# Performance work log

Hardware: AMD Instinct MI355X
Metric: run time of the kernel (lower is better)

## Reference

```python
import jax, jax.numpy as jnp
import numpy as np

B, T, D = 2, 2048, 1024
QH, KVH = 16, 4
HD = D // QH          # 64
G = QH // KVH         # group size 4
SCALE = HD ** -0.5


def _rope_rotate(x):
    # interleaved rotation: (x1, x2) -> (-x2, x1)
    x1 = x[..., ::2]
    x2 = x[..., 1::2]
    return jnp.stack((-x2, x1), axis=-1).reshape(x.shape)


def setup_inputs() -> dict:
    key = jax.random.key(0)
    k0, k1, k2, k3 = jax.random.split(key, 4)
    x = jax.random.normal(k0, (B, T, D), dtype=jnp.float32)
    # proper RoPE tables, shape [T, HD], each frequency repeated for the interleaved pair
    inv_freq = 1.0 / (10000.0 ** (np.arange(0, HD, 2, dtype=np.float32) / HD))
    freqs = np.arange(T, dtype=np.float32)[:, None] * inv_freq[None, :]   # [T, HD/2]
    freqs = np.repeat(freqs, 2, axis=-1)                                   # [T, HD]
    cos = jnp.asarray(np.cos(freqs), dtype=jnp.float32)
    sin = jnp.asarray(np.sin(freqs), dtype=jnp.float32)
    # glorot-uniform weights stored torch-style as [out, in]
    def glorot(k, out_d, in_d):
        lim = float(np.sqrt(6.0 / (in_d + out_d)))
        return jax.random.uniform(k, (out_d, in_d), jnp.float32, -lim, lim)
    Wq = glorot(k1, D, D)
    Wkv = glorot(k2, 2 * KVH * HD, D)
    Wo = glorot(k3, D, D)
    return {"x": x, "cos": cos, "sin": sin, "Wq": Wq, "Wkv": Wkv, "Wo": Wo}


def reference(x, cos, sin, Wq, Wkv, Wo):
    # projections (torch Linear: y = x @ W.T)
    q = (x @ Wq.T).reshape(B, T, QH, HD).transpose(0, 2, 1, 3)        # [B,QH,T,HD]
    kv = (x @ Wkv.T).reshape(B, T, KVH, 2, HD)
    k = kv[..., 0, :].transpose(0, 2, 1, 3)                            # [B,KVH,T,HD]
    v = kv[..., 1, :].transpose(0, 2, 1, 3)                            # [B,KVH,T,HD]
    # inline RoPE (cos/sin broadcast over batch & heads)
    q = q * cos + _rope_rotate(q) * sin
    k = k * cos + _rope_rotate(k) * sin
    # GQA via broadcast instead of repeat_interleave (same math)
    qg = q.reshape(B, KVH, G, T, HD)
    scores = jnp.einsum('bkgtd,bksd->bkgts', qg, k) * SCALE            # [B,KVH,G,T,T]
    attn = jax.nn.softmax(scores, axis=-1)  # dropout is identity in eval
    out = jnp.einsum('bkgts,bksd->bkgtd', attn, v)                     # [B,KVH,G,T,HD]
    out = out.reshape(B, QH, T, HD).transpose(0, 2, 1, 3).reshape(B, T, D)
    return out @ Wo.T
```

## Files before the change

### kernel.cpp

```cpp
#include <hip/hip_runtime.h>


typedef __bf16 bf16x8 __attribute__((ext_vector_type(8)));
typedef float f32x4 __attribute__((ext_vector_type(4)));
typedef float f32x16 __attribute__((ext_vector_type(16)));
typedef int i32x4 __attribute__((ext_vector_type(4)));
typedef unsigned short ushort4v __attribute__((ext_vector_type(4)));
typedef unsigned short ushort8v __attribute__((ext_vector_type(8)));
typedef unsigned short u16;
typedef unsigned int u32;

#define DEVINL __device__ __forceinline__

DEVINL float bf2f(u16 u) {
  unsigned int x = ((unsigned int)u) << 16;
  return __builtin_bit_cast(float, x);
}
DEVINL u16 f2bf(float f) {
  unsigned int x = __builtin_bit_cast(unsigned int, f);
  x += 0x7fffu + ((x >> 16) & 1u);
  return (u16)(x >> 16);
}
DEVINL float exp2r(float x) {
  float r;
  asm("v_exp_f32 %0, %1" : "=v"(r) : "v"(x));
  return r;
}

constexpr int Bb = 2, Tt = 2048, Dd = 1024, QH = 16, KVH = 4, HD = 64;
constexpr float SCALE_L2E = 0.125f * 1.44269504088896340736f;
constexpr int KVSZ = 131072;

__global__ void cvt_all(const float* __restrict__ x, const float* __restrict__ Wq,
                        const float* __restrict__ Wkv, const float* __restrict__ Wo,
                        u16* __restrict__ xb, u16* __restrict__ wqkv,
                        u16* __restrict__ wob) {
  int i = blockIdx.x * 256 + threadIdx.x;
  const float* src;
  u16* dst;
  if (i < 1048576) {
    src = x; dst = xb;
  } else if (i < 1310720) {
    src = Wq - (size_t)1048576 * 4; dst = wqkv - (size_t)1048576 * 4;
  } else if (i < 1441792) {
    src = Wkv - (size_t)1310720 * 4; dst = wqkv + (size_t)1024 * 1024 - (size_t)1310720 * 4;
  } else {
    src = Wo - (size_t)1441792 * 4; dst = wob - (size_t)1441792 * 4;
  }
  float4 v = reinterpret_cast<const float4*>(src)[i];
  ushort4v o = {f2bf(v.x), f2bf(v.y), f2bf(v.z), f2bf(v.w)};
  *reinterpret_cast<ushort4v*>(dst + (size_t)i * 4) = o;
}

template <bool OUT_F32>
__global__ __launch_bounds__(256) void gemm_bt(const u16* __restrict__ A,
                                               const u16* __restrict__ Bw,
                                               void* __restrict__ Cout, int M, int N, int K) {
  __shared__ alignas(16) u16 lA[128 * 64];
  __shared__ alignas(16) u16 lB[128 * 64];
  const int tid = threadIdx.x;
  const int w = tid >> 6, lane = tid & 63;
  const int r16 = lane & 15, g4 = lane >> 4;
  const int row0 = blockIdx.y * 128, col0 = blockIdx.x * 128;
  const int sr = tid >> 3, sc = tid & 7;
  const int NT = K >> 6;

  bf16x8 ra[4], rb[4];
  f32x4 acc[4][4];
#pragma unroll
  for (int i = 0; i < 4; ++i)
#pragma unroll
    for (int j = 0; j < 4; ++j) acc[i][j] = f32x4{0.f, 0.f, 0.f, 0.f};

  const int wm = (w >> 1) * 64, wn = (w & 1) * 64;

#pragma unroll
  for (int i = 0; i < 4; ++i) {
    int r = i * 32 + sr;
    ra[i] = *reinterpret_cast<const bf16x8*>(A + (size_t)(row0 + r) * K + sc * 8);
    rb[i] = *reinterpret_cast<const bf16x8*>(Bw + (size_t)(col0 + r) * K + sc * 8);
  }

  for (int kt = 0; kt < NT; ++kt) {
    __syncthreads();
#pragma unroll
    for (int i = 0; i < 4; ++i) {
      int r = i * 32 + sr;
      int c = (sc ^ (r & 7)) * 8;
      *reinterpret_cast<bf16x8*>(&lA[r * 64 + c]) = ra[i];
      *reinterpret_cast<bf16x8*>(&lB[r * 64 + c]) = rb[i];
    }
    __syncthreads();
    if (kt + 1 < NT) {
      int k0 = (kt + 1) << 6;
#pragma unroll
      for (int i = 0; i < 4; ++i) {
        int r = i * 32 + sr;
        ra[i] = *reinterpret_cast<const bf16x8*>(A + (size_t)(row0 + r) * K + k0 + sc * 8);
        rb[i] = *reinterpret_cast<const bf16x8*>(Bw + (size_t)(col0 + r) * K + k0 + sc * 8);
      }
    }
#pragma unroll
    for (int kk = 0; kk < 2; ++kk) {
      bf16x8 af[4], bfr[4];
#pragma unroll
      for (int mf = 0; mf < 4; ++mf) {
        int r = wm + mf * 16 + r16;
        int c = ((kk * 4 + g4) ^ (r & 7)) * 8;
        af[mf] = *reinterpret_cast<const bf16x8*>(&lA[r * 64 + c]);
      }
#pragma unroll
      for (int nf = 0; nf < 4; ++nf) {
        int r = wn + nf * 16 + r16;
        int c = ((kk * 4 + g4) ^ (r & 7)) * 8;
        bfr[nf] = *reinterpret_cast<const bf16x8*>(&lB[r * 64 + c]);
      }
#pragma unroll
      for (int mf = 0; mf < 4; ++mf)
#pragma unroll
        for (int nf = 0; nf < 4; ++nf)
          acc[mf][nf] =
              __builtin_amdgcn_mfma_f32_16x16x32_bf16(af[mf], bfr[nf], acc[mf][nf], 0, 0, 0);
    }
  }

#pragma unroll
  for (int mf = 0; mf < 4; ++mf)
#pragma unroll
    for (int nf = 0; nf < 4; ++nf)
#pragma unroll
      for (int r = 0; r < 4; ++r) {
        size_t row = (size_t)(row0 + wm + mf * 16 + g4 * 4 + r);
        size_t col = (size_t)(col0 + wn + nf * 16 + r16);
        float v = acc[mf][nf][r];
        if (OUT_F32)
          reinterpret_cast<float*>(Cout)[row * N + col] = v;
        else
          reinterpret_cast<u16*>(Cout)[row * N + col] = f2bf(v);
      }
}

__global__ void rope_scatter(const u16* __restrict__ P, const float* __restrict__ cosT,
                             const float* __restrict__ sinT, u16* __restrict__ Q,
                             u16* __restrict__ Kc) {
  int idx = blockIdx.x * 256 + threadIdx.x;
  if (idx >= (Bb * Tt) * 640) return;
  int row = idx / 640, p = idx - row * 640;
  int b = row >> 11, t = row & 2047;
  int n, d;
  u16* outp;
  float scl;
  if (p < 512) {
    n = p * 2;
    int h = n >> 6;
    d = n & 63;
    outp = Q + ((size_t)(b * QH + h) * Tt + t) * HD + d;
    scl = SCALE_L2E;
  } else {
    int r2 = p - 512;
    int kvh = r2 >> 5, dp = r2 & 31;
    d = dp * 2;
    n = 1024 + kvh * 128 + d;
    int bh = b * KVH + kvh;
    int kf = d >> 4, h8 = (d >> 3) & 1, j = d & 7;
    outp = Kc + (size_t)bh * KVSZ + ((t >> 5) * 4 + kf) * 512 + (h8 * 32 + (t & 31)) * 8 + j;
    scl = 1.0f;
  }
  unsigned int pv = *reinterpret_cast<const unsigned int*>(P + (size_t)row * 1536 + n);
  float v0 = bf2f((u16)(pv & 0xffffu)), v1 = bf2f((u16)(pv >> 16));
  float c = cosT[t * HD + d], s = sinT[t * HD + d];
  float o0 = (v0 * c - v1 * s) * scl;
  float o1 = (v1 * c + v0 * s) * scl;
  unsigned int ob = (unsigned int)f2bf(o0) | ((unsigned int)f2bf(o1) << 16);
  *reinterpret_cast<unsigned int*>(outp) = ob;
}

__global__ void v_transpose(const u16* __restrict__ P, u16* __restrict__ Vf) {
  __shared__ u16 tile[64][72];
  int bh = blockIdx.y;
  int b = bh >> 2, kvh = bh & 3;
  int t0 = blockIdx.x * 64;
  int tid = threadIdx.x;
  int colbase = 1024 + kvh * 128 + 64;
#pragma unroll
  for (int j = 0; j < 4; ++j) {
    int rr = j * 16 + (tid >> 4);
    int cc = (tid & 15) * 4;
    *reinterpret_cast<uint2*>(&tile[rr][cc]) =
        *reinterpret_cast<const uint2*>(P + (size_t)(b * Tt + t0 + rr) * 1536 + colbase + cc);
  }
  __syncthreads();
#pragma unroll
  for (int kk = 0; kk < 2; ++kk) {
    int CH = kk * 256 + tid;
    int df = CH >> 8, sbks = (CH >> 6) & 3, h8 = (CH >> 5) & 1, l = CH & 31;
    int d = df * 32 + l;
    int c = (sbks >> 1) * 4 + (sbks & 1) * 2 + h8;
    ushort8v v;
#pragma unroll
    for (int j = 0; j < 8; ++j) v[j] = tile[c * 8 + j][d];
    u16* dst = Vf + (size_t)bh * KVSZ + (((t0 >> 6) * 2 + df) * 4 + sbks) * 512 +
               (h8 * 32 + l) * 8;
    *reinterpret_cast<ushort8v*>(dst) = v;
  }
}

__global__ __launch_bounds__(512, 4) void attn_fwd7(const u16* __restrict__ Q,
                                                    const u16* __restrict__ Kf,
                                                    const u16* __restrict__ Vf,
                                                    u16* __restrict__ Oa) {
  __shared__ alignas(16) float cmb[2][32][66];
  __shared__ alignas(16) u16 ot[2][32][72];
  const int tid = threadIdx.x;
  const int w = tid >> 6, lane = tid & 63;
  const int qsub = w & 1, spl = w >> 1;
  const int l31 = lane & 31, hi = lane >> 5;

  const int fid = blockIdx.x;
  const int xcd = fid & 7, idx = fid >> 3;
  const int b = xcd >> 2, kvh = xcd & 3;
  const int g = idx & 3, qblk = idx >> 2;
  const int h = kvh * 4 + g;
  const int t0 = qblk * 64 + qsub * 32;

  const u16* Qh = Q + ((size_t)(b * QH + h) * Tt + t0 + l31) * HD + hi * 8;
  const u16* Kp = Kf + (size_t)(b * KVH + kvh) * KVSZ + lane * 8 + (size_t)spl * 32768;
  const u16* Vp = Vf + (size_t)(b * KVH + kvh) * KVSZ + lane * 8 + (size_t)spl * 32768;

  bf16x8 qf[4];
#pragma unroll
  for (int kf = 0; kf < 4; ++kf)
    qf[kf] = *reinterpret_cast<const bf16x8*>(Qh + kf * 16);

  f32x16 oacc[2];
#pragma unroll
  for (int df = 0; df < 2; ++df)
#pragma unroll
    for (int r = 0; r < 16; ++r) oacc[df][r] = 0.f;
  float lp = 0.f;

  for (int it = 0; it < 8; ++it, Kp += 4096, Vp += 4096) {
    f32x16 sacc[2];
#pragma unroll
    for (int sb = 0; sb < 2; ++sb) {
      bf16x8 kfr[4];
#pragma unroll
      for (int kf = 0; kf < 4; ++kf)
        kfr[kf] = *reinterpret_cast<const bf16x8*>(Kp + sb * 2048 + kf * 512);
#pragma unroll
      for (int r = 0; r < 16; ++r) sacc[sb][r] = 0.f;
      __builtin_amdgcn_s_setprio(1);
#pragma unroll
      for (int kf = 0; kf < 4; ++kf)
        sacc[sb] = __builtin_amdgcn_mfma_f32_32x32x16_bf16(kfr[kf], qf[kf], sacc[sb], 0, 0, 0);
      __builtin_amdgcn_s_setprio(0);
    }

    float a0 = 0.f, a1 = 0.f, a2 = 0.f, a3 = 0.f;
#pragma unroll
    for (int sb = 0; sb < 2; ++sb)
#pragma unroll
      for (int r = 0; r < 16; r += 4) {
        float e0 = exp2r(sacc[sb][r]);
        float e1 = exp2r(sacc[sb][r + 1]);
        float e2 = exp2r(sacc[sb][r + 2]);
        float e3 = exp2r(sacc[sb][r + 3]);
        sacc[sb][r] = e0; sacc[sb][r + 1] = e1; sacc[sb][r + 2] = e2; sacc[sb][r + 3] = e3;
        a0 += e0; a1 += e1; a2 += e2; a3 += e3;
      }
    lp += (a0 + a1) + (a2 + a3);

    bf16x8 pf[2][2];
#pragma unroll
    for (int sb = 0; sb < 2; ++sb) {
      u32 pw[8];
#pragma unroll
      for (int r2 = 0; r2 < 8; ++r2) {
        u32 o;
        asm("v_cvt_pk_bf16_f32 %0, %1, %2"
            : "=v"(o)
            : "v"(sacc[sb][2 * r2]), "v"(sacc[sb][2 * r2 + 1]));
        pw[r2] = o;
      }
      u32 fw[2][4];
#pragma unroll
      for (int pp = 0; pp < 4; ++pp) {
        int ks = pp >> 1, o = pp & 1;
        u32 a = pw[ks * 4 + o], bq = pw[ks * 4 + o + 2];
        asm("v_permlane32_swap_b32 %0, %1" : "+v"(a), "+v"(bq));
        fw[ks][o] = a;
        fw[ks][o + 2] = bq;
      }
#pragma unroll
      for (int ks = 0; ks < 2; ++ks) {
        i32x4 iv = {(int)fw[ks][0], (int)fw[ks][1], (int)fw[ks][2], (int)fw[ks][3]};
        pf[sb][ks] = __builtin_bit_cast(bf16x8, iv);
      }
    }

    bf16x8 vf[2][2][2];
#pragma unroll
    for (int df = 0; df < 2; ++df)
#pragma unroll
      for (int sb = 0; sb < 2; ++sb)
#pragma unroll
        for (int ks = 0; ks < 2; ++ks)
          vf[df][sb][ks] =
              *reinterpret_cast<const bf16x8*>(Vp + (size_t)(df * 4 + sb * 2 + ks) * 512);

    __builtin_amdgcn_s_setprio(1);
#pragma unroll
    for (int df = 0; df < 2; ++df)
#pragma unroll
      for (int sb = 0; sb < 2; ++sb)
#pragma unroll
        for (int ks = 0; ks < 2; ++ks)
          oacc[df] =
              __builtin_amdgcn_mfma_f32_32x32x16_bf16(vf[df][sb][ks], pf[sb][ks], oacc[df], 0, 0, 0);
    __builtin_amdgcn_s_setprio(0);
  }

  lp += __shfl_xor(lp, 32);

  for (int src = 1; src < 4; ++src) {
    if (spl == src) {
      float* cb = &cmb[qsub][l31][0];
#pragma unroll
      for (int df = 0; df < 2; ++df)
#pragma unroll
        for (int r = 0; r < 16; ++r) {
          int d = df * 32 + (r & 3) + 8 * (r >> 2) + 4 * hi;
          cb[d] = oacc[df][r];
        }
      if (hi == 0) cb[64] = lp;
    }
    __syncthreads();
    if (spl == 0) {
      const float* cb = &cmb[qsub][l31][0];
      lp += cb[64];
#pragma unroll
      for (int df = 0; df < 2; ++df)
#pragma unroll
        for (int r = 0; r < 16; ++r) {
          int d = df * 32 + (r & 3) + 8 * (r >> 2) + 4 * hi;
          oacc[df][r] += cb[d];
        }
    }
    __syncthreads();
  }

  if (spl == 0) {
    float linv = 1.0f / lp;
#pragma unroll
    for (int df = 0; df < 2; ++df)
#pragma unroll
      for (int r = 0; r < 16; ++r) {
        int d = df * 32 + (r & 3) + 8 * (r >> 2) + 4 * hi;
        ot[qsub][l31][d] = f2bf(oacc[df][r] * linv);
      }
  }
  __syncthreads();
  if (spl == 0) {
    int tr = lane >> 1, dblk = (lane & 1) * 32;
    u16* gdst = Oa + ((size_t)(b * Tt + t0 + tr)) * Dd + h * HD + dblk;
#pragma unroll
    for (int c = 0; c < 4; ++c) {
      ushort8v vv = *reinterpret_cast<const ushort8v*>(&ot[qsub][tr][dblk + c * 8]);
      *reinterpret_cast<ushort8v*>(gdst + c * 8) = vv;
    }
  }
}

extern "C" void kernel_launch(void* const* d_in, const int* in_sizes, int n_in, void* d_out,
                              int out_size, void* d_ws, size_t ws_size, hipStream_t stream) {
  (void)in_sizes; (void)n_in; (void)out_size; (void)ws_size;
  const float* x = (const float*)d_in[0];
  const float* cosT = (const float*)d_in[1];
  const float* sinT = (const float*)d_in[2];
  const float* Wq = (const float*)d_in[3];
  const float* Wkv = (const float*)d_in[4];
  const float* Wo = (const float*)d_in[5];

  char* p = (char*)d_ws;
  u16* xb = (u16*)p;   p += (size_t)4096 * 1024 * 2;
  u16* wqkv = (u16*)p; p += (size_t)1536 * 1024 * 2;
  u16* wob = (u16*)p;  p += (size_t)1024 * 1024 * 2;
  u16* Pbuf = (u16*)p; p += (size_t)4096 * 1536 * 2;
  u16* Qb = (u16*)p;   p += (size_t)Bb * QH * Tt * HD * 2;
  u16* Kbuf = (u16*)p; p += (size_t)Bb * KVH * Tt * HD * 2;
  u16* Vfb = (u16*)p;  p += (size_t)Bb * KVH * HD * Tt * 2;
  u16* Ob = Pbuf;

  cvt_all<<<6656, 256, 0, stream>>>(x, Wq, Wkv, Wo, xb, wqkv, wob);
  gemm_bt<false><<<dim3(12, 32), 256, 0, stream>>>(xb, wqkv, Pbuf, 4096, 1536, 1024);
  rope_scatter<<<10240, 256, 0, stream>>>(Pbuf, cosT, sinT, Qb, Kbuf);
  v_transpose<<<dim3(32, 8), 256, 0, stream>>>(Pbuf, Vfb);
  attn_fwd7<<<1024, 512, 0, stream>>>(Qb, Kbuf, Vfb, Ob);
  gemm_bt<true><<<dim3(8, 32), 256, 0, stream>>>(Ob, wob, d_out, 4096, 1024, 1024);
}
```

Measured before the change: 109.9 us.

## Load GEMM tiles directly into LDS and prefetch K/V early in attention

The bf16 GEMM now stages A/B tiles with global_load_lds straight into LDS instead of going through registers. This drops the register-held next-tile prefetch and the XOR swizzle of the LDS layout. The attention kernel preloads K fragments for the next iteration and issues V loads right after the QK MFMAs, so memory latency overlaps with the softmax work. The trade-off is that the GEMM now has unswizzled LDS reads, which can cause bank conflicts, and no software pipelining between loads and compute. The attention change costs extra registers for the prefetched K.

```diff
diff --git a/kernel.cpp b/kernel.cpp
--- a/kernel.cpp
+++ b/kernel.cpp
@@ -25,6 +25,11 @@
   float r;
   asm("v_exp_f32 %0, %1" : "=v"(r) : "v"(x));
   return r;
+}
+DEVINL void gld16(const u16* g, u16* l) {
+  __builtin_amdgcn_global_load_lds(
+      (const __attribute__((address_space(1))) void*)g,
+      (__attribute__((address_space(3))) void*)l, 16, 0, 0);
 }
 
 constexpr int Bb = 2, Tt = 2048, Dd = 1024, QH = 16, KVH = 4, HD = 64;
@@ -64,57 +69,39 @@
   const int row0 = blockIdx.y * 128, col0 = blockIdx.x * 128;
   const int sr = tid >> 3, sc = tid & 7;
   const int NT = K >> 6;
-
-  bf16x8 ra[4], rb[4];
+  const int wm = (w >> 1) * 64, wn = (w & 1) * 64;
+
   f32x4 acc[4][4];
 #pragma unroll
   for (int i = 0; i < 4; ++i)
 #pragma unroll
     for (int j = 0; j < 4; ++j) acc[i][j] = f32x4{0.f, 0.f, 0.f, 0.f};
 
-  const int wm = (w >> 1) * 64, wn = (w & 1) * 64;
-
-#pragma unroll
-  for (int i = 0; i < 4; ++i) {
-    int r = i * 32 + sr;
-    ra[i] = *reinterpret_cast<const bf16x8*>(A + (size_t)(row0 + r) * K + sc * 8);
-    rb[i] = *reinterpret_cast<const bf16x8*>(Bw + (size_t)(col0 + r) * K + sc * 8);
-  }
+  const u16* Ap = A + (size_t)(row0 + sr) * K + sc * 8;
+  const u16* Bp = Bw + (size_t)(col0 + sr) * K + sc * 8;
+  u16* lAb = &lA[(size_t)(w * 8) * 64];
+  u16* lBb = &lB[(size_t)(w * 8) * 64];
 
   for (int kt = 0; kt < NT; ++kt) {
     __syncthreads();
+    const int k0 = kt << 6;
 #pragma unroll
     for (int i = 0; i < 4; ++i) {
-      int r = i * 32 + sr;
-      int c = (sc ^ (r & 7)) * 8;
-      *reinterpret_cast<bf16x8*>(&lA[r * 64 + c]) = ra[i];
-      *reinterpret_cast<bf16x8*>(&lB[r * 64 + c]) = rb[i];
+      gld16(Ap + (size_t)(i * 32) * K + k0, lAb + i * 32 * 64);
+      gld16(Bp + (size_t)(i * 32) * K + k0, lBb + i * 32 * 64);
     }
     __syncthreads();
-    if (kt + 1 < NT) {
-      int k0 = (kt + 1) << 6;
-#pragma unroll
-      for (int i = 0; i < 4; ++i) {
-        int r = i * 32 + sr;
-        ra[i] = *reinterpret_cast<const bf16x8*>(A + (size_t)(row0 + r) * K + k0 + sc * 8);
-        rb[i] = *reinterpret_cast<const bf16x8*>(Bw + (size_t)(col0 + r) * K + k0 + sc * 8);
-      }
-    }
 #pragma unroll
     for (int kk = 0; kk < 2; ++kk) {
       bf16x8 af[4], bfr[4];
 #pragma unroll
-      for (int mf = 0; mf < 4; ++mf) {
-        int r = wm + mf * 16 + r16;
-        int c = ((kk * 4 + g4) ^ (r & 7)) * 8;
-        af[mf] = *reinterpret_cast<const bf16x8*>(&lA[r * 64 + c]);
-      }
-#pragma unroll
-      for (int nf = 0; nf < 4; ++nf) {
-        int r = wn + nf * 16 + r16;
-        int c = ((kk * 4 + g4) ^ (r & 7)) * 8;
-        bfr[nf] = *reinterpret_cast<const bf16x8*>(&lB[r * 64 + c]);
-      }
+      for (int mf = 0; mf < 4; ++mf)
+        af[mf] = *reinterpret_cast<const bf16x8*>(
+            &lA[(wm + mf * 16 + r16) * 64 + (kk * 4 + g4) * 8]);
+#pragma unroll
+      for (int nf = 0; nf < 4; ++nf)
+        bfr[nf] = *reinterpret_cast<const bf16x8*>(
+            &lB[(wn + nf * 16 + r16) * 64 + (kk * 4 + g4) * 8]);
 #pragma unroll
       for (int mf = 0; mf < 4; ++mf)
 #pragma unroll
@@ -205,7 +192,7 @@
   }
 }
 
-__global__ __launch_bounds__(512, 4) void attn_fwd7(const u16* __restrict__ Q,
+__global__ __launch_bounds__(512, 4) void attn_fwd8(const u16* __restrict__ Q,
                                                     const u16* __restrict__ Kf,
                                                     const u16* __restrict__ Vf,
                                                     u16* __restrict__ Oa) {
@@ -239,21 +226,45 @@
     for (int r = 0; r < 16; ++r) oacc[df][r] = 0.f;
   float lp = 0.f;
 
+  bf16x8 kfr[2][4];
+#pragma unroll
+  for (int sb = 0; sb < 2; ++sb)
+#pragma unroll
+    for (int kf = 0; kf < 4; ++kf)
+      kfr[sb][kf] = *reinterpret_cast<const bf16x8*>(Kp + sb * 2048 + kf * 512);
+
   for (int it = 0; it < 8; ++it, Kp += 4096, Vp += 4096) {
     f32x16 sacc[2];
 #pragma unroll
     for (int sb = 0; sb < 2; ++sb) {
-      bf16x8 kfr[4];
+#pragma unroll
+      for (int r = 0; r < 16; ++r) sacc[sb][r] = 0.f;
+    }
+    __builtin_amdgcn_s_setprio(1);
+#pragma unroll
+    for (int sb = 0; sb < 2; ++sb)
 #pragma unroll
       for (int kf = 0; kf < 4; ++kf)
-        kfr[kf] = *reinterpret_cast<const bf16x8*>(Kp + sb * 2048 + kf * 512);
-#pragma unroll
-      for (int r = 0; r < 16; ++r) sacc[sb][r] = 0.f;
-      __builtin_amdgcn_s_setprio(1);
-#pragma unroll
-      for (int kf = 0; kf < 4; ++kf)
-        sacc[sb] = __builtin_amdgcn_mfma_f32_32x32x16_bf16(kfr[kf], qf[kf], sacc[sb], 0, 0, 0);
-      __builtin_amdgcn_s_setprio(0);
+        sacc[sb] = __builtin_amdgcn_mfma_f32_32x32x16_bf16(kfr[sb][kf], qf[kf], sacc[sb], 0, 0, 0);
+    __builtin_amdgcn_s_setprio(0);
+
+    bf16x8 vf[2][2][2];
+#pragma unroll
+    for (int df = 0; df < 2; ++df)
+#pragma unroll
+      for (int sb = 0; sb < 2; ++sb)
+#pragma unroll
+        for (int ks = 0; ks < 2; ++ks)
+          vf[df][sb][ks] =
+              *reinterpret_cast<const bf16x8*>(Vp + (size_t)(df * 4 + sb * 2 + ks) * 512);
+
+    if (it < 7) {
+#pragma unroll
+      for (int sb = 0; sb < 2; ++sb)
+#pragma unroll
+        for (int kf = 0; kf < 4; ++kf)
+          kfr[sb][kf] =
+              *reinterpret_cast<const bf16x8*>(Kp + 4096 + sb * 2048 + kf * 512);
     }
 
     float a0 = 0.f, a1 = 0.f, a2 = 0.f, a3 = 0.f;
@@ -297,16 +308,6 @@
         pf[sb][ks] = __builtin_bit_cast(bf16x8, iv);
       }
     }
-
-    bf16x8 vf[2][2][2];
-#pragma unroll
-    for (int df = 0; df < 2; ++df)
-#pragma unroll
-      for (int sb = 0; sb < 2; ++sb)
-#pragma unroll
-        for (int ks = 0; ks < 2; ++ks)
-          vf[df][sb][ks] =
-              *reinterpret_cast<const bf16x8*>(Vp + (size_t)(df * 4 + sb * 2 + ks) * 512);
 
     __builtin_amdgcn_s_setprio(1);
 #pragma unroll
@@ -395,6 +396,6 @@
   gemm_bt<false><<<dim3(12, 32), 256, 0, stream>>>(xb, wqkv, Pbuf, 4096, 1536, 1024);
   rope_scatter<<<10240, 256, 0, stream>>>(Pbuf, cosT, sinT, Qb, Kbuf);
   v_transpose<<<dim3(32, 8), 256, 0, stream>>>(Pbuf, Vfb);
-  attn_fwd7<<<1024, 512, 0, stream>>>(Qb, Kbuf, Vfb, Ob);
+  attn_fwd8<<<1024, 512, 0, stream>>>(Qb, Kbuf, Vfb, Ob);
   gemm_bt<true><<<dim3(8, 32), 256, 0, stream>>>(Ob, wob, d_out, 4096, 1024, 1024);
 }
```

Result: slower. 180.8 us (+64.5%).
